# Kernel tuning notes

Measured on AMD Instinct MI355X. Metric: run time of the kernel, lower is better.

Reference implementation:

```python
import jax, jax.numpy as jnp
import numpy as np

B, N, E, C = 8, 4096, 1024, 512


def setup_inputs() -> dict:
    key = jax.random.key(0)
    k1, k2, k3, k4 = jax.random.split(key, 4)
    node_feats = jax.random.normal(k1, (B, N, C), dtype=jnp.float32)
    hyper_feats = jax.random.normal(k2, (B, E, C), dtype=jnp.float32)
    # torch nn.Linear params: weight [out, in], bias [out]
    Wq = jax.random.normal(k3, (C, C), dtype=jnp.float32) * (1.0 / np.sqrt(C))
    bq = jnp.zeros((C,), dtype=jnp.float32)
    Wkv = jax.random.normal(k4, (2 * C, C), dtype=jnp.float32) * (1.0 / np.sqrt(C))
    bkv = jnp.zeros((2 * C,), dtype=jnp.float32)
    return {"node_feats": node_feats, "hyper_feats": hyper_feats,
            "Wq": Wq, "bq": bq, "Wkv": Wkv, "bkv": bkv}


def reference(node_feats, hyper_feats, Wq, bq, Wkv, bkv):
    C_ = node_feats.shape[-1]
    scale = C_ ** -0.5
    Q = node_feats @ Wq.T + bq                      # [B,N,C]
    KV = hyper_feats @ Wkv.T + bkv                  # [B,E,2C]
    K, V = KV[..., :C_], KV[..., C_:]               # [B,E,C] each
    attn = jnp.einsum('bnc,bec->bne', Q, K) * scale  # [B,N,E]
    attn = jax.nn.softmax(attn, axis=-1)
    return jnp.einsum('bne,bec->bnc', attn, V)       # [B,N,C]
```

## Files before the change

### kernel.cpp

```cpp
#include <hip/hip_runtime.h>
#include <cstdint>
#include <cstddef>

typedef _Float16 h16;
typedef _Float16 h16x4 __attribute__((ext_vector_type(4)));
typedef _Float16 h16x8 __attribute__((ext_vector_type(8)));
typedef float fx4 __attribute__((ext_vector_type(4)));

static constexpr int B_ = 8, N_ = 4096, E_ = 1024, C_ = 512;
static constexpr float SCALE = 0.044194173824159216f;

__device__ __forceinline__ void glds16(const h16* g, h16* l) {
  __builtin_amdgcn_global_load_lds(
      (const __attribute__((address_space(1))) unsigned int*)g,
      (__attribute__((address_space(3))) unsigned int*)l, 16, 0, 0);
}

__global__ __launch_bounds__(256) void cvt_kernel(const float* __restrict__ src,
                                                  h16* __restrict__ dst, int n8) {
  int i = blockIdx.x * 256 + threadIdx.x;
  if (i >= n8) return;
  const float4* s4 = (const float4*)src;
  float4 a = s4[2 * i], b = s4[2 * i + 1];
  h16x8 o;
  o[0] = (h16)a.x; o[1] = (h16)a.y; o[2] = (h16)a.z; o[3] = (h16)a.w;
  o[4] = (h16)b.x; o[5] = (h16)b.y; o[6] = (h16)b.z; o[7] = (h16)b.w;
  *(h16x8*)(dst + (size_t)i * 8) = o;
}

template <int MODE>
__global__ __launch_bounds__(256) void gemm_bt(
    const h16* __restrict__ Ah, const h16* __restrict__ Bm,
    const float* __restrict__ bias,
    h16* __restrict__ outH, h16* __restrict__ outK, h16* __restrict__ outVt,
    float* __restrict__ outF, float* __restrict__ rowsum,
    int Ncols, int K) {
  __shared__ h16 sA[128 * 32];
  __shared__ h16 sB[128 * 32];
  const int tid = threadIdx.x;
  const int wave = tid >> 6, lane = tid & 63;
  const int wm = wave >> 1, wn = wave & 1;
  const int lr = lane & 15, kq = lane >> 4;
  const int mBase = blockIdx.x * 128, nBase = blockIdx.y * 128;
  const int z = blockIdx.z;
  if (MODE == 2) { Ah += (size_t)z * N_ * C_; Bm += (size_t)z * E_ * C_;
                   outH += (size_t)z * N_ * E_; rowsum += (size_t)z * N_; }
  if (MODE == 3) { Ah += (size_t)z * N_ * E_; Bm += (size_t)z * C_ * E_;
                   outF += (size_t)z * N_ * C_; rowsum += (size_t)z * N_; }

  fx4 acc[4][4];
#pragma unroll
  for (int i = 0; i < 4; i++)
#pragma unroll
    for (int j = 0; j < 4; j++) acc[i][j] = (fx4){0.f, 0.f, 0.f, 0.f};

  const int rowInA = lane >> 2, colInA = (lane & 3) * 8;

  for (int kb = 0; kb < K; kb += 32) {
    __syncthreads();
#pragma unroll
    for (int i = 0; i < 2; i++) {
      int chunk = wave + i * 4;
      glds16(Ah + (size_t)(mBase + chunk * 16 + rowInA) * K + kb + colInA,
             &sA[chunk * 512]);
      glds16(Bm + (size_t)(nBase + chunk * 16 + rowInA) * K + kb + colInA,
             &sB[chunk * 512]);
    }
    __syncthreads();
    h16x8 af[4], bf[4];
#pragma unroll
    for (int mi = 0; mi < 4; mi++)
      af[mi] = *(const h16x8*)&sA[(wm * 64 + mi * 16 + lr) * 32 + kq * 8];
#pragma unroll
    for (int ni = 0; ni < 4; ni++)
      bf[ni] = *(const h16x8*)&sB[(wn * 64 + ni * 16 + lr) * 32 + kq * 8];
#pragma unroll
    for (int mi = 0; mi < 4; mi++)
#pragma unroll
      for (int ni = 0; ni < 4; ni++)
        acc[mi][ni] = __builtin_amdgcn_mfma_f32_16x16x32_f16(af[mi], bf[ni], acc[mi][ni], 0, 0, 0);
  }

  const int rb = kq * 4;
  if (MODE == 2) {
#pragma unroll
    for (int mi = 0; mi < 4; mi++) {
#pragma unroll
      for (int r = 0; r < 4; r++) {
        int row = mBase + wm * 64 + mi * 16 + rb + r;
        float rs = 0.f;
#pragma unroll
        for (int ni = 0; ni < 4; ni++) {
          int col = nBase + wn * 64 + ni * 16 + lr;
          float e = __expf(acc[mi][ni][r] * SCALE);
          rs += e;
          outH[(size_t)row * Ncols + col] = (h16)e;
        }
        rs += __shfl_xor(rs, 1); rs += __shfl_xor(rs, 2);
        rs += __shfl_xor(rs, 4); rs += __shfl_xor(rs, 8);
        if (lr == 0) atomicAdd(&rowsum[row], rs);
      }
    }
  } else if (MODE == 3) {
#pragma unroll
    for (int mi = 0; mi < 4; mi++) {
#pragma unroll
      for (int r = 0; r < 4; r++) {
        int row = mBase + wm * 64 + mi * 16 + rb + r;
        float inv = 1.0f / rowsum[row];
#pragma unroll
        for (int ni = 0; ni < 4; ni++) {
          int col = nBase + wn * 64 + ni * 16 + lr;
          outF[(size_t)row * Ncols + col] = acc[mi][ni][r] * inv;
        }
      }
    }
  } else {
#pragma unroll
    for (int mi = 0; mi < 4; mi++) {
#pragma unroll
      for (int ni = 0; ni < 4; ni++) {
        int row0 = mBase + wm * 64 + mi * 16 + rb;
        int col = nBase + wn * 64 + ni * 16 + lr;
        if (MODE == 1 && col >= C_) {
          float bv = bias[col];
          h16x4 pk;
#pragma unroll
          for (int r = 0; r < 4; r++) pk[r] = (h16)(acc[mi][ni][r] + bv);
          int zb = row0 >> 10, e = row0 & 1023;
          *(h16x4*)&outVt[((size_t)zb * C_ + (col - C_)) * E_ + e] = pk;
        } else {
#pragma unroll
          for (int r = 0; r < 4; r++) {
            int row = row0 + r;
            float v = acc[mi][ni][r] + bias[col];
            if (MODE == 0) outH[(size_t)row * Ncols + col] = (h16)v;
            else           outK[(size_t)row * C_ + col] = (h16)v;
          }
        }
      }
    }
  }
}

extern "C" void kernel_launch(void* const* d_in, const int* in_sizes, int n_in,
                              void* d_out, int out_size, void* d_ws, size_t ws_size,
                              hipStream_t stream) {
  const float* node  = (const float*)d_in[0];
  const float* hyper = (const float*)d_in[1];
  const float* Wq    = (const float*)d_in[2];
  const float* bq    = (const float*)d_in[3];
  const float* Wkv   = (const float*)d_in[4];
  const float* bkv   = (const float*)d_in[5];
  float* out = (float*)d_out;
  char* ws = (char*)d_ws;

  h16* node_h  = (h16*)(ws + 0);
  h16* hyper_h = (h16*)(ws + 33554432);
  h16* S_h     = (h16*)(ws + 0);
  h16* Q_h     = (h16*)(ws + 67108864);
  h16* K_h     = (h16*)(ws + 100663296);
  h16* Vt_h    = (h16*)(ws + 109051904);
  h16* Wq_h    = (h16*)(ws + 117440512);
  h16* Wkv_h   = (h16*)(ws + 117964800);
  float* rowsum = (float*)(ws + 119013376);
  if (ws_size < 119144448u) return;

  cvt_kernel<<<dim3((B_ * N_ * C_ / 8 + 255) / 256), 256, 0, stream>>>(node, node_h, B_ * N_ * C_ / 8);
  cvt_kernel<<<dim3((B_ * E_ * C_ / 8 + 255) / 256), 256, 0, stream>>>(hyper, hyper_h, B_ * E_ * C_ / 8);
  cvt_kernel<<<dim3((C_ * C_ / 8 + 255) / 256), 256, 0, stream>>>(Wq, Wq_h, C_ * C_ / 8);
  cvt_kernel<<<dim3((2 * C_ * C_ / 8 + 255) / 256), 256, 0, stream>>>(Wkv, Wkv_h, 2 * C_ * C_ / 8);
  hipMemsetAsync(rowsum, 0, (size_t)B_ * N_ * sizeof(float), stream);

  gemm_bt<0><<<dim3(B_ * N_ / 128, C_ / 128), 256, 0, stream>>>(
      node_h, Wq_h, bq, Q_h, nullptr, nullptr, nullptr, nullptr, C_, C_);
  gemm_bt<1><<<dim3(B_ * E_ / 128, 2 * C_ / 128), 256, 0, stream>>>(
      hyper_h, Wkv_h, bkv, nullptr, K_h, Vt_h, nullptr, nullptr, 2 * C_, C_);
  gemm_bt<2><<<dim3(N_ / 128, E_ / 128, B_), 256, 0, stream>>>(
      Q_h, K_h, nullptr, S_h, nullptr, nullptr, nullptr, rowsum, E_, C_);
  gemm_bt<3><<<dim3(N_ / 128, C_ / 128, B_), 256, 0, stream>>>(
      S_h, Vt_h, nullptr, nullptr, nullptr, nullptr, out, rowsum, C_, E_);
}
```

Baseline: 315.6 us.

## Fuse QK^T, exp, and PV into a single flash-style attention kernel

Replaces the separate score GEMM (writing an fp16 exp(S) matrix to global memory with atomic rowsums) and the PV GEMM with one kernel that keeps each 128-row query block's exp scores in LDS and accumulates the output in registers across E tiles. Row sums are reduced in shared memory at the end, which removes the memset and the global atomics. The goal is to drop the large B*N*E intermediate write and read-back and two launches. In exchange, Q is re-streamed from global for every E tile, K and V are loaded straight from global without LDS staging, and there is no max-subtraction, same as before.

```diff
diff --git a/kernel.cpp b/kernel.cpp
--- a/kernel.cpp
+++ b/kernel.cpp
@@ -33,7 +33,6 @@
     const h16* __restrict__ Ah, const h16* __restrict__ Bm,
     const float* __restrict__ bias,
     h16* __restrict__ outH, h16* __restrict__ outK, h16* __restrict__ outVt,
-    float* __restrict__ outF, float* __restrict__ rowsum,
     int Ncols, int K) {
   __shared__ h16 sA[128 * 32];
   __shared__ h16 sB[128 * 32];
@@ -42,11 +41,6 @@
   const int wm = wave >> 1, wn = wave & 1;
   const int lr = lane & 15, kq = lane >> 4;
   const int mBase = blockIdx.x * 128, nBase = blockIdx.y * 128;
-  const int z = blockIdx.z;
-  if (MODE == 2) { Ah += (size_t)z * N_ * C_; Bm += (size_t)z * E_ * C_;
-                   outH += (size_t)z * N_ * E_; rowsum += (size_t)z * N_; }
-  if (MODE == 3) { Ah += (size_t)z * N_ * E_; Bm += (size_t)z * C_ * E_;
-                   outF += (size_t)z * N_ * C_; rowsum += (size_t)z * N_; }
 
   fx4 acc[4][4];
 #pragma unroll
@@ -82,65 +76,171 @@
   }
 
   const int rb = kq * 4;
-  if (MODE == 2) {
+#pragma unroll
+  for (int mi = 0; mi < 4; mi++) {
+#pragma unroll
+    for (int ni = 0; ni < 4; ni++) {
+      int row0 = mBase + wm * 64 + mi * 16 + rb;
+      int col = nBase + wn * 64 + ni * 16 + lr;
+      if (MODE == 1 && col >= C_) {
+        float bv = bias[col];
+        h16x4 pk;
+#pragma unroll
+        for (int r = 0; r < 4; r++) pk[r] = (h16)(acc[mi][ni][r] + bv);
+        int zb = row0 >> 10, e = row0 & 1023;
+        *(h16x4*)&outVt[((size_t)zb * C_ + (col - C_)) * E_ + e] = pk;
+      } else {
+#pragma unroll
+        for (int r = 0; r < 4; r++) {
+          int row = row0 + r;
+          float v = acc[mi][ni][r] + bias[col];
+          if (MODE == 0) outH[(size_t)row * Ncols + col] = (h16)v;
+          else           outK[(size_t)row * C_ + col] = (h16)v;
+        }
+      }
+    }
+  }
+}
+
+__global__ __launch_bounds__(512) void flash_attn(
+    const h16* __restrict__ Qm, const h16* __restrict__ Km,
+    const h16* __restrict__ Vtm, float* __restrict__ out) {
+  __shared__ h16 qbuf[2][4096];
+  __shared__ h16 Pb[128 * 136];
+  const int tid = threadIdx.x;
+  const int wave = tid >> 6, lane = tid & 63;
+  const int lr = lane & 15, kq = lane >> 4;
+  const int z = blockIdx.x;
+  const int mBase = blockIdx.y * 128;
+  const h16* Qb = Qm + ((size_t)z * N_ + mBase) * C_;
+  const h16* Kb = Km + (size_t)z * E_ * C_;
+  const h16* Vb = Vtm + (size_t)z * C_ * E_;
+  float* outb = out + ((size_t)z * N_ + mBase) * C_;
+
+  const int sm = wave >> 2, sn = wave & 3;
+  const int pm = wave >> 2, pc = wave & 3;
+
+  fx4 Oacc[4][8];
+#pragma unroll
+  for (int i = 0; i < 4; i++)
+#pragma unroll
+    for (int j = 0; j < 8; j++) Oacc[i][j] = (fx4){0.f, 0.f, 0.f, 0.f};
+  float rsp[4][4];
+#pragma unroll
+  for (int i = 0; i < 4; i++)
+#pragma unroll
+    for (int r = 0; r < 4; r++) rsp[i][r] = 0.f;
+
+  const int qRow = wave * 16 + (lane >> 2);
+  const int qCol = (lane & 3) * 8;
+
+  glds16(Qb + (size_t)qRow * C_ + 0 + qCol, &qbuf[0][wave * 512]);
+
+#pragma unroll 1
+  for (int et = 0; et < 8; ++et) {
+    const int e0 = et * 128;
+    fx4 Sacc[4][2];
 #pragma unroll
     for (int mi = 0; mi < 4; mi++) {
-#pragma unroll
-      for (int r = 0; r < 4; r++) {
-        int row = mBase + wm * 64 + mi * 16 + rb + r;
-        float rs = 0.f;
-#pragma unroll
-        for (int ni = 0; ni < 4; ni++) {
-          int col = nBase + wn * 64 + ni * 16 + lr;
-          float e = __expf(acc[mi][ni][r] * SCALE);
-          rs += e;
-          outH[(size_t)row * Ncols + col] = (h16)e;
-        }
-        rs += __shfl_xor(rs, 1); rs += __shfl_xor(rs, 2);
-        rs += __shfl_xor(rs, 4); rs += __shfl_xor(rs, 8);
-        if (lr == 0) atomicAdd(&rowsum[row], rs);
-      }
-    }
-  } else if (MODE == 3) {
-#pragma unroll
-    for (int mi = 0; mi < 4; mi++) {
-#pragma unroll
-      for (int r = 0; r < 4; r++) {
-        int row = mBase + wm * 64 + mi * 16 + rb + r;
-        float inv = 1.0f / rowsum[row];
-#pragma unroll
-        for (int ni = 0; ni < 4; ni++) {
-          int col = nBase + wn * 64 + ni * 16 + lr;
-          outF[(size_t)row * Ncols + col] = acc[mi][ni][r] * inv;
-        }
-      }
-    }
-  } else {
-#pragma unroll
-    for (int mi = 0; mi < 4; mi++) {
-#pragma unroll
-      for (int ni = 0; ni < 4; ni++) {
-        int row0 = mBase + wm * 64 + mi * 16 + rb;
-        int col = nBase + wn * 64 + ni * 16 + lr;
-        if (MODE == 1 && col >= C_) {
-          float bv = bias[col];
-          h16x4 pk;
-#pragma unroll
-          for (int r = 0; r < 4; r++) pk[r] = (h16)(acc[mi][ni][r] + bv);
-          int zb = row0 >> 10, e = row0 & 1023;
-          *(h16x4*)&outVt[((size_t)zb * C_ + (col - C_)) * E_ + e] = pk;
-        } else {
-#pragma unroll
-          for (int r = 0; r < 4; r++) {
-            int row = row0 + r;
-            float v = acc[mi][ni][r] + bias[col];
-            if (MODE == 0) outH[(size_t)row * Ncols + col] = (h16)v;
-            else           outK[(size_t)row * C_ + col] = (h16)v;
-          }
-        }
-      }
+      Sacc[mi][0] = (fx4){0.f, 0.f, 0.f, 0.f};
+      Sacc[mi][1] = (fx4){0.f, 0.f, 0.f, 0.f};
+    }
+    const h16* Kw0 = Kb + (size_t)(e0 + sn * 32 + lr) * C_ + kq * 8;
+    const h16* Kw1 = Kw0 + (size_t)16 * C_;
+    h16x8 kf0 = *(const h16x8*)Kw0;
+    h16x8 kf1 = *(const h16x8*)Kw1;
+#pragma unroll 1
+    for (int kc = 0; kc < 16; ++kc) {
+      __syncthreads();
+      if (!(et == 7 && kc == 15))
+        glds16(Qb + (size_t)qRow * C_ + (((kc + 1) & 15) * 32) + qCol,
+               &qbuf[(kc + 1) & 1][wave * 512]);
+      if (kc < 15) {
+        h16x8 kn0 = *(const h16x8*)(Kw0 + (kc + 1) * 32);
+        h16x8 kn1 = *(const h16x8*)(Kw1 + (kc + 1) * 32);
+        h16x8 af[4];
+        const h16* qb = &qbuf[kc & 1][0];
+#pragma unroll
+        for (int mi = 0; mi < 4; mi++)
+          af[mi] = *(const h16x8*)&qb[(sm * 64 + mi * 16 + lr) * 32 + kq * 8];
+#pragma unroll
+        for (int mi = 0; mi < 4; mi++) {
+          Sacc[mi][0] = __builtin_amdgcn_mfma_f32_16x16x32_f16(af[mi], kf0, Sacc[mi][0], 0, 0, 0);
+          Sacc[mi][1] = __builtin_amdgcn_mfma_f32_16x16x32_f16(af[mi], kf1, Sacc[mi][1], 0, 0, 0);
+        }
+        kf0 = kn0; kf1 = kn1;
+      } else {
+        h16x8 af[4];
+        const h16* qb = &qbuf[kc & 1][0];
+#pragma unroll
+        for (int mi = 0; mi < 4; mi++)
+          af[mi] = *(const h16x8*)&qb[(sm * 64 + mi * 16 + lr) * 32 + kq * 8];
+#pragma unroll
+        for (int mi = 0; mi < 4; mi++) {
+          Sacc[mi][0] = __builtin_amdgcn_mfma_f32_16x16x32_f16(af[mi], kf0, Sacc[mi][0], 0, 0, 0);
+          Sacc[mi][1] = __builtin_amdgcn_mfma_f32_16x16x32_f16(af[mi], kf1, Sacc[mi][1], 0, 0, 0);
+        }
+      }
+    }
+#pragma unroll
+    for (int mi = 0; mi < 4; mi++)
+#pragma unroll
+      for (int ni = 0; ni < 2; ni++) {
+        int col = sn * 32 + ni * 16 + lr;
+#pragma unroll
+        for (int r = 0; r < 4; r++) {
+          int row = sm * 64 + mi * 16 + kq * 4 + r;
+          float e = __expf(Sacc[mi][ni][r] * SCALE);
+          rsp[mi][r] += e;
+          Pb[row * 136 + col] = (h16)e;
+        }
+      }
+    __syncthreads();
+#pragma unroll 1
+    for (int kc = 0; kc < 4; ++kc) {
+      h16x8 vf[8];
+#pragma unroll
+      for (int ni = 0; ni < 8; ni++)
+        vf[ni] = *(const h16x8*)(Vb + (size_t)(pc * 128 + ni * 16 + lr) * E_ +
+                                 e0 + kc * 32 + kq * 8);
+      h16x8 pf[4];
+#pragma unroll
+      for (int mi = 0; mi < 4; mi++)
+        pf[mi] = *(const h16x8*)&Pb[(pm * 64 + mi * 16 + lr) * 136 + kc * 32 + kq * 8];
+#pragma unroll
+      for (int mi = 0; mi < 4; mi++)
+#pragma unroll
+        for (int ni = 0; ni < 8; ni++)
+          Oacc[mi][ni] = __builtin_amdgcn_mfma_f32_16x16x32_f16(pf[mi], vf[ni], Oacc[mi][ni], 0, 0, 0);
     }
   }
+
+  __syncthreads();
+  float* rs = (float*)&qbuf[0][0];
+  if (tid < 128) rs[tid] = 0.f;
+  __syncthreads();
+#pragma unroll
+  for (int mi = 0; mi < 4; mi++)
+#pragma unroll
+    for (int r = 0; r < 4; r++) {
+      float v = rsp[mi][r];
+      v += __shfl_xor(v, 1); v += __shfl_xor(v, 2);
+      v += __shfl_xor(v, 4); v += __shfl_xor(v, 8);
+      if (lr == 0) atomicAdd(&rs[sm * 64 + mi * 16 + kq * 4 + r], v);
+    }
+  __syncthreads();
+#pragma unroll
+  for (int mi = 0; mi < 4; mi++)
+#pragma unroll
+    for (int r = 0; r < 4; r++) {
+      int row = pm * 64 + mi * 16 + kq * 4 + r;
+      float inv = 1.0f / rs[row];
+#pragma unroll
+      for (int ni = 0; ni < 8; ni++) {
+        int col = pc * 128 + ni * 16 + lr;
+        outb[(size_t)row * C_ + col] = Oacc[mi][ni][r] * inv;
+      }
+    }
 }
 
 extern "C" void kernel_launch(void* const* d_in, const int* in_sizes, int n_in,
@@ -157,27 +257,21 @@
 
   h16* node_h  = (h16*)(ws + 0);
   h16* hyper_h = (h16*)(ws + 33554432);
-  h16* S_h     = (h16*)(ws + 0);
-  h16* Q_h     = (h16*)(ws + 67108864);
-  h16* K_h     = (h16*)(ws + 100663296);
-  h16* Vt_h    = (h16*)(ws + 109051904);
-  h16* Wq_h    = (h16*)(ws + 117440512);
-  h16* Wkv_h   = (h16*)(ws + 117964800);
-  float* rowsum = (float*)(ws + 119013376);
-  if (ws_size < 119144448u) return;
+  h16* Q_h     = (h16*)(ws + 41943040);
+  h16* K_h     = (h16*)(ws + 75497472);
+  h16* Vt_h    = (h16*)(ws + 83886080);
+  h16* Wq_h    = (h16*)(ws + 92274688);
+  h16* Wkv_h   = (h16*)(ws + 92798976);
+  if (ws_size < 93847552u) return;
 
   cvt_kernel<<<dim3((B_ * N_ * C_ / 8 + 255) / 256), 256, 0, stream>>>(node, node_h, B_ * N_ * C_ / 8);
   cvt_kernel<<<dim3((B_ * E_ * C_ / 8 + 255) / 256), 256, 0, stream>>>(hyper, hyper_h, B_ * E_ * C_ / 8);
   cvt_kernel<<<dim3((C_ * C_ / 8 + 255) / 256), 256, 0, stream>>>(Wq, Wq_h, C_ * C_ / 8);
   cvt_kernel<<<dim3((2 * C_ * C_ / 8 + 255) / 256), 256, 0, stream>>>(Wkv, Wkv_h, 2 * C_ * C_ / 8);
-  hipMemsetAsync(rowsum, 0, (size_t)B_ * N_ * sizeof(float), stream);
 
   gemm_bt<0><<<dim3(B_ * N_ / 128, C_ / 128), 256, 0, stream>>>(
-      node_h, Wq_h, bq, Q_h, nullptr, nullptr, nullptr, nullptr, C_, C_);
+      node_h, Wq_h, bq, Q_h, nullptr, nullptr, C_, C_);
   gemm_bt<1><<<dim3(B_ * E_ / 128, 2 * C_ / 128), 256, 0, stream>>>(
-      hyper_h, Wkv_h, bkv, nullptr, K_h, Vt_h, nullptr, nullptr, 2 * C_, C_);
-  gemm_bt<2><<<dim3(N_ / 128, E_ / 128, B_), 256, 0, stream>>>(
-      Q_h, K_h, nullptr, S_h, nullptr, nullptr, nullptr, rowsum, E_, C_);
-  gemm_bt<3><<<dim3(N_ / 128, C_ / 128, B_), 256, 0, stream>>>(
-      S_h, Vt_h, nullptr, nullptr, nullptr, nullptr, out, rowsum, C_, E_);
-}
+      hyper_h, Wkv_h, bkv, nullptr, K_h, Vt_h, 2 * C_, C_);
+  flash_attn<<<dim3(B_, N_ / 128), 512, 0, stream>>>(Q_h, K_h, Vt_h, out);
+}
```

Result: slower. 373.6 us (+18.4%).
